# Performance work log

Hardware: AMD Instinct MI355X
Metric: run time of the kernel (lower is better)

Reference implementation:

```python
import jax, jax.numpy as jnp
import numpy as np
import math

B, L, D = 8, 2048, 256


def setup_inputs() -> dict:
    key = jax.random.key(0)
    ks = jax.random.split(key, 8)
    return {
        "query": jax.random.normal(ks[0], (B, L, D), dtype=jnp.float32),
        "key": jax.random.normal(ks[1], (B, L, D), dtype=jnp.float32),
        "value": jax.random.normal(ks[2], (B, L, D), dtype=jnp.float32),
        "mask": jax.random.randint(ks[3], (B, L), 0, 2, dtype=jnp.int32),
        "Wq_w": jax.random.normal(ks[4], (D, D), dtype=jnp.float32) * 0.05,
        "Wq_b": jax.random.normal(ks[5], (D,), dtype=jnp.float32) * 0.05,
        "Wk_w": jax.random.normal(ks[6], (D, D), dtype=jnp.float32) * 0.05,
        "Wk_b": jax.random.normal(ks[7], (D,), dtype=jnp.float32) * 0.05,
    }


def reference(query, key, value, mask, Wq_w, Wq_b, Wk_w, Wk_b):
    d = query.shape[-1]
    q = query @ Wq_w.T + Wq_b            # [B, Lq, D]
    k = key @ Wk_w.T + Wk_b              # [B, Lk, D]
    scores = jnp.einsum("bqd,bkd->bqk", q, k) / math.sqrt(d)  # [B, Lq, Lk]
    m = mask.astype(scores.dtype)[:, None, :]                  # [B, 1, Lk]
    # multiplicative then additive masking, as in original
    scores = jnp.where(m == 0, jnp.asarray(-1e9, scores.dtype), scores * m)
    attn = jax.nn.softmax(scores, axis=-1)
    return jnp.einsum("bqk,bkd->bqd", attn, value)
```

## Files before the change

kernel.cpp:

```cpp
#include <hip/hip_runtime.h>
#include <stdint.h>
#include <stddef.h>

#define B_ 8
#define L_ 2048
#define D_ 256
#define KSPLIT 4
#define KRANGE 512
#define KTILE 32
#define NITER 16

typedef __bf16 bf16x8 __attribute__((ext_vector_type(8)));
typedef float floatx4 __attribute__((ext_vector_type(4)));
typedef float floatx16 __attribute__((ext_vector_type(16)));
typedef _Float16 half4_t __attribute__((ext_vector_type(4)));

__device__ __forceinline__ short f2bf(float f) {
    union { float f; uint32_t u; } v; v.f = f;
    return (short)((v.u + 0x8000u) >> 16);
}

__device__ __forceinline__ uint32_t pack2bf(float a, float b) {
    union { float f; uint32_t u; } x, y; x.f = a; y.f = b;
    return ((x.u + 0x8000u) >> 16) | ((y.u + 0x8000u) & 0xFFFF0000u);
}

__device__ __forceinline__ uint32_t cvtpk_bf16(float lo, float hi2) {
    uint32_t w;
    asm("v_cvt_pk_bf16_f32 %0, %1, %2" : "=v"(w) : "v"(lo), "v"(hi2));
    return w;
}

__device__ __forceinline__ void pl32swap(uint32_t &a, uint32_t &b) {
    asm("v_permlane32_swap_b32 %0, %1" : "+v"(a), "+v"(b));
}

__device__ __forceinline__ void async16(const void* g, void* l) {
    __builtin_amdgcn_global_load_lds(
        (__attribute__((address_space(1))) void*)g,
        (__attribute__((address_space(3))) void*)l,
        16, 0, 0);
}

__global__ __launch_bounds__(256, 3) void prep_kernel(
    const float* __restrict__ Xq, const float* __restrict__ Xk,
    const float* __restrict__ Wq, const float* __restrict__ Wk,
    const float* __restrict__ bq, const float* __restrict__ bk,
    const float* __restrict__ V,
    short* __restrict__ Oq, short* __restrict__ Ok, short* __restrict__ Vt)
{
    __shared__ uint32_t shm[2 * 64 * 20 + 2 * 256 * 20];
    const int bid = blockIdx.x;
    const int tid = threadIdx.x;

    if (bid & 1) {
        uint32_t* T = shm;
        const int vb = bid >> 1;
        const int b  = vb >> 6;
        const int l0 = (vb & 63) * 32;
        const int r2 = tid >> 4;
        const int dg = tid & 15;
        const int lp = r2 ^ ((dg & 3) << 2);
#pragma unroll
        for (int p = 0; p < 4; p++) {
            int d0 = (dg + p * 16) * 4;
            const float* src = V + ((size_t)b * L_ + l0 + r2 * 2) * D_ + d0;
            float4 e0 = *(const float4*)src;
            float4 e1 = *(const float4*)(src + D_);
            T[(d0 + 0) * 20 + lp] = pack2bf(e0.x, e1.x);
            T[(d0 + 1) * 20 + lp] = pack2bf(e0.y, e1.y);
            T[(d0 + 2) * 20 + lp] = pack2bf(e0.z, e1.z);
            T[(d0 + 3) * 20 + lp] = pack2bf(e0.w, e1.w);
        }
        __syncthreads();
#pragma unroll
        for (int p = 0; p < 4; p++) {
            int d = (tid >> 2) + p * 64;
            int c = tid & 3;
            int cp = c ^ ((d >> 2) & 3);
            uint4 u = *(const uint4*)&T[d * 20 + cp * 4];
            *(uint4*)(Vt + ((size_t)b * D_ + d) * L_ + l0 + c * 8) = u;
        }
        return;
    }

    const int pb = bid >> 1;
    const int py = pb >> 8;
    const int px = pb & 255;

    const float* X    = py ? Xk : Xq;
    const float* W    = py ? Wk : Wq;
    const float* bias = py ? bk : bq;
    short* Out        = py ? Ok : Oq;

    uint32_t* As = shm;
    uint32_t* Ws = shm + 2 * 64 * 20;

    const int wid  = tid >> 6;
    const int lane = tid & 63;
    const int m16  = lane & 15;
    const int quad = lane >> 4;
    const int row0 = px * 64;
    const int ar = tid >> 2, cg = tid & 3;

    floatx4 acc[16];
    const floatx4 z4 = {0.f, 0.f, 0.f, 0.f};
#pragma unroll
    for (int i = 0; i < 16; i++) acc[i] = z4;

    {
        const float* srcA = X + (size_t)(row0 + ar) * D_ + cg * 8;
        float4 a = *(const float4*)srcA, b2 = *(const float4*)(srcA + 4);
        uint4 u; u.x = pack2bf(a.x, a.y); u.y = pack2bf(a.z, a.w);
        u.z = pack2bf(b2.x, b2.y); u.w = pack2bf(b2.z, b2.w);
        *(uint4*)&As[ar * 20 + cg * 4] = u;
#pragma unroll
        for (int p = 0; p < 4; p++) {
            const float* srcW = W + (size_t)(p * 64 + ar) * D_ + cg * 8;
            float4 wa = *(const float4*)srcW, wb = *(const float4*)(srcW + 4);
            uint4 w; w.x = pack2bf(wa.x, wa.y); w.y = pack2bf(wa.z, wa.w);
            w.z = pack2bf(wb.x, wb.y); w.w = pack2bf(wb.z, wb.w);
            *(uint4*)&Ws[(p * 64 + ar) * 20 + cg * 4] = w;
        }
    }
    __syncthreads();

    for (int kc = 0; kc < 8; kc++) {
        const int buf = kc & 1;
        float4 na, nb, nwa[4], nwb[4];
        if (kc < 7) {
            const int k1 = (kc + 1) * 32;
            const float* srcA = X + (size_t)(row0 + ar) * D_ + k1 + cg * 8;
            na = *(const float4*)srcA; nb = *(const float4*)(srcA + 4);
#pragma unroll
            for (int p = 0; p < 4; p++) {
                const float* srcW = W + (size_t)(p * 64 + ar) * D_ + k1 + cg * 8;
                nwa[p] = *(const float4*)srcW; nwb[p] = *(const float4*)(srcW + 4);
            }
        }
        bf16x8 af = *(const bf16x8*)&As[buf * 1280 + (wid * 16 + m16) * 20 + quad * 4];
#pragma unroll
        for (int n = 0; n < 16; n++) {
            bf16x8 bfr = *(const bf16x8*)&Ws[buf * 5120 + (n * 16 + m16) * 20 + quad * 4];
            acc[n] = __builtin_amdgcn_mfma_f32_16x16x32_bf16(af, bfr, acc[n], 0, 0, 0);
        }
        if (kc < 7) {
            uint4 u; u.x = pack2bf(na.x, na.y); u.y = pack2bf(na.z, na.w);
            u.z = pack2bf(nb.x, nb.y); u.w = pack2bf(nb.z, nb.w);
            *(uint4*)&As[(buf ^ 1) * 1280 + ar * 20 + cg * 4] = u;
#pragma unroll
            for (int p = 0; p < 4; p++) {
                uint4 w; w.x = pack2bf(nwa[p].x, nwa[p].y); w.y = pack2bf(nwa[p].z, nwa[p].w);
                w.z = pack2bf(nwb[p].x, nwb[p].y); w.w = pack2bf(nwb[p].z, nwb[p].w);
                *(uint4*)&Ws[(buf ^ 1) * 5120 + (p * 64 + ar) * 20 + cg * 4] = w;
            }
        }
        __syncthreads();
    }
#pragma unroll
    for (int n = 0; n < 16; n++) {
        const int col = n * 16 + m16;
        const float bv = bias[col];
#pragma unroll
        for (int r = 0; r < 4; r++) {
            const int row = row0 + wid * 16 + quad * 4 + r;
            Out[(size_t)row * D_ + col] = f2bf(acc[n][r] + bv);
        }
    }
}

__global__ __launch_bounds__(256, 2) void flash_kernel(
    const short* __restrict__ Qb, const short* __restrict__ Kb,
    const short* __restrict__ Vt, const int* __restrict__ mask,
    float* __restrict__ Out, _Float16* __restrict__ Part,
    float* __restrict__ Lpart)
{
    __shared__ short Ks[2][KTILE * 256];
    __shared__ short Vs[2][256 * KTILE];

    const int tid  = threadIdx.x;
    const int wid  = tid >> 6;
    const int lane = tid & 63;
    const int l31  = lane & 31;
    const int hi   = lane >> 5;
    const int b  = blockIdx.x;
    const int q0 = blockIdx.y * 128;
    const int z  = blockIdx.z;

    const char* kgb = (const char*)(Kb + ((size_t)b * L_ + z * KRANGE) * D_);
    const char* vgb = (const char*)(Vt + (size_t)b * D_ * L_ + z * KRANGE);
    const int*  mg  = mask + b * L_ + z * KRANGE;

    bf16x8 qf[16];
    {
        const short* qrow = Qb + ((size_t)b * L_ + q0 + wid * 32 + l31) * D_ + hi * 8;
#pragma unroll
        for (int dt = 0; dt < 16; dt++)
            qf[dt] = *(const bf16x8*)(qrow + dt * 16);
    }

    uint32_t mbits = 0;
#pragma unroll
    for (int t = 0; t < NITER; t++)
        mbits |= (mg[t * KTILE + l31] != 0 ? 1u : 0u) << t;

    floatx16 o[8];
#pragma unroll
    for (int n = 0; n < 8; n++)
#pragma unroll
        for (int r = 0; r < 16; r++) o[n][r] = 0.f;
    float rsum = 0.f;

    const int KBb = l31 * 512 + ((((l31 & 7) ^ ((l31 >> 3) & 3)) ^ hi) << 4);
    const int VBb = l31 * 64 + (((((l31 >> 1) & 3) ^ ((l31 >> 3) & 1)) ^ hi) << 4);

    int koff[4], voff[4];
#pragma unroll
    for (int c = 0; c < 4; c++) {
        int row = wid * 8 + c * 2 + hi;
        int gk = l31 ^ (row & 7) ^ ((row >> 3) & 3);
        koff[c] = row * 512 + gk * 16;
        int d = (wid * 4 + c) * 16 + (lane >> 2);
        int gv = (lane & 3) ^ ((lane >> 3) & 3) ^ ((lane >> 5) & 1);
        voff[c] = d * (L_ * 2) + gv * 16;
    }

#pragma unroll
    for (int c = 0; c < 4; c++)
        async16(kgb + koff[c], &Ks[0][0] + (wid * 4 + c) * 512);
#pragma unroll
    for (int c = 0; c < 4; c++)
        async16(vgb + voff[c], &Vs[1][0] + (wid * 4 + c) * 512);
    __builtin_amdgcn_s_waitcnt(0x0F70);
    __syncthreads();

    const float C2 = 0.09016844f;
    bf16x8 pfA, pfB;
    {
        union { uint32_t u[4]; bf16x8 v; } zz;
        zz.u[0] = 0; zz.u[1] = 0; zz.u[2] = 0; zz.u[3] = 0;
        pfA = zz.v; pfB = zz.v;
    }

    for (int t2 = 0; t2 < NITER; t2 += 2) {
#pragma unroll
        for (int half = 0; half < 2; half++) {
            const int t = t2 + half;
            const int buf = half;

            {
                const char* kp = kgb + (size_t)(t + 1) * (KTILE * D_ * 2);
                const char* vp = vgb + (size_t)t * (KTILE * 2);
#pragma unroll
                for (int c = 0; c < 4; c++)
                    async16(kp + koff[c], &Ks[buf ^ 1][0] + (wid * 4 + c) * 512);
#pragma unroll
                for (int c = 0; c < 4; c++)
                    async16(vp + voff[c], &Vs[buf][0] + (wid * 4 + c) * 512);
            }

            const char* kl = (const char*)&Ks[buf][0];
            floatx16 s0, s1;
#pragma unroll
            for (int r = 0; r < 16; r++) { s0[r] = 0.f; s1[r] = 0.f; }
            __builtin_amdgcn_s_setprio(1);
#pragma unroll
            for (int dt = 0; dt < 16; dt += 2) {
                bf16x8 kf0 = *(const bf16x8*)(kl + (KBb ^ (dt << 5)));
                bf16x8 kf1 = *(const bf16x8*)(kl + (KBb ^ ((dt + 1) << 5)));
                s0 = __builtin_amdgcn_mfma_f32_32x32x16_bf16(kf0, qf[dt], s0, 0, 0, 0);
                s1 = __builtin_amdgcn_mfma_f32_32x32x16_bf16(kf1, qf[dt + 1], s1, 0, 0, 0);
            }

            const char* vl = (const char*)&Vs[buf ^ 1][0];
#pragma unroll
            for (int n = 0; n < 8; n++) {
                bf16x8 vf0 = *(const bf16x8*)(vl + (VBb ^ (n << 11)));
                bf16x8 vf1 = *(const bf16x8*)(vl + (VBb ^ ((n << 11) | 32)));
                o[n] = __builtin_amdgcn_mfma_f32_32x32x16_bf16(pfA, vf0, o[n], 0, 0, 0);
                o[n] = __builtin_amdgcn_mfma_f32_32x32x16_bf16(pfB, vf1, o[n], 0, 0, 0);
            }
            __builtin_amdgcn_s_setprio(0);

            uint32_t mb = (uint32_t)__ballot((mbits >> t) & 1) >> (hi * 4);
            uint32_t w[8];
#pragma unroll
            for (int i = 0; i < 8; i++) {
                const int r0 = 2 * i, r1 = 2 * i + 1;
                const int k0 = (r0 & 3) + 8 * (r0 >> 2);
                float sv0 = s0[r0] + s1[r0];
                float sv1 = s0[r1] + s1[r1];
                float e0 = ((mb >> k0) & 1) ? exp2f(sv0 * C2) : 0.f;
                float e1 = ((mb >> (k0 + 1)) & 1) ? exp2f(sv1 * C2) : 0.f;
                rsum += e0 + e1;
                w[i] = cvtpk_bf16(e0, e1);
            }
            pl32swap(w[0], w[2]); pl32swap(w[1], w[3]);
            pl32swap(w[4], w[6]); pl32swap(w[5], w[7]);
            {
                union { uint32_t u[4]; bf16x8 v; } ua, ub;
                ua.u[0] = w[0]; ua.u[1] = w[1]; ua.u[2] = w[2]; ua.u[3] = w[3];
                ub.u[0] = w[4]; ub.u[1] = w[5]; ub.u[2] = w[6]; ub.u[3] = w[7];
                pfA = ua.v; pfB = ub.v;
            }

            __syncthreads();
        }
    }

    {
        const char* vl = (const char*)&Vs[1][0];
        __builtin_amdgcn_s_setprio(1);
#pragma unroll
        for (int n = 0; n < 8; n++) {
            bf16x8 vf0 = *(const bf16x8*)(vl + (VBb ^ (n << 11)));
            bf16x8 vf1 = *(const bf16x8*)(vl + (VBb ^ ((n << 11) | 32)));
            o[n] = __builtin_amdgcn_mfma_f32_32x32x16_bf16(pfA, vf0, o[n], 0, 0, 0);
            o[n] = __builtin_amdgcn_mfma_f32_32x32x16_bf16(pfB, vf1, o[n], 0, 0, 0);
        }
        __builtin_amdgcn_s_setprio(0);
    }

    rsum += __shfl_xor(rsum, 32);

    const size_t BLD = (size_t)B_ * L_ * D_;
    const size_t rowbase = (size_t)b * L_ + q0 + wid * 32;
    if (z == 0) {
        float* po = Out + rowbase * D_;
#pragma unroll
        for (int n = 0; n < 8; n++)
#pragma unroll
            for (int r = 0; r < 16; r++) {
                int q = (r & 3) + 8 * (r >> 2) + 4 * hi;
                po[(size_t)q * D_ + n * 32 + l31] = o[n][r];
            }
    } else {
        _Float16* pp = Part + (size_t)(z - 1) * BLD + rowbase * D_;
#pragma unroll
        for (int n = 0; n < 8; n++)
#pragma unroll
            for (int r = 0; r < 16; r++) {
                int q = (r & 3) + 8 * (r >> 2) + 4 * hi;
                pp[(size_t)q * D_ + n * 32 + l31] = (_Float16)o[n][r];
            }
    }
    if (lane < 32) {
        Lpart[(size_t)z * (B_ * L_) + rowbase + lane] = rsum;
    }
}

__global__ __launch_bounds__(256) void norm_kernel(
    float* __restrict__ Out, const _Float16* __restrict__ Part,
    const float* __restrict__ Lpart)
{
    const int idx = blockIdx.x * 256 + threadIdx.x;
    const int row = idx >> 6;
    const int c   = (idx & 63) * 4;
    const size_t off = (size_t)row * D_ + c;
    const size_t BLD = (size_t)B_ * L_ * D_;
    float4 acc = *(float4*)(Out + off);
#pragma unroll
    for (int zz = 0; zz < 3; zz++) {
        half4_t h = *(const half4_t*)(Part + zz * BLD + off);
        acc.x += (float)h.x; acc.y += (float)h.y;
        acc.z += (float)h.z; acc.w += (float)h.w;
    }
    const int BL = B_ * L_;
    float l = Lpart[row] + Lpart[BL + row] + Lpart[2 * BL + row] + Lpart[3 * BL + row];
    float inv = 1.0f / l;
    acc.x *= inv; acc.y *= inv; acc.z *= inv; acc.w *= inv;
    *(float4*)(Out + off) = acc;
}

extern "C" void kernel_launch(void* const* d_in, const int* in_sizes, int n_in,
                              void* d_out, int out_size, void* d_ws, size_t ws_size,
                              hipStream_t stream) {
    const float* query = (const float*)d_in[0];
    const float* key   = (const float*)d_in[1];
    const float* value = (const float*)d_in[2];
    const int*   mask  = (const int*)d_in[3];
    const float* Wq_w  = (const float*)d_in[4];
    const float* Wq_b  = (const float*)d_in[5];
    const float* Wk_w  = (const float*)d_in[6];
    const float* Wk_b  = (const float*)d_in[7];
    float* out = (float*)d_out;

    const size_t BLD = (size_t)B_ * L_ * D_;
    short* qb = (short*)d_ws;
    short* kb = qb + BLD;
    short* vt = kb + BLD;
    _Float16* part = (_Float16*)(vt + BLD);
    float* lpart = (float*)(part + 3 * BLD);

    prep_kernel<<<dim3(1024), 256, 0, stream>>>(query, key, Wq_w, Wk_w, Wq_b, Wk_b,
                                                value, qb, kb, vt);
    flash_kernel<<<dim3(8, 16, 4), 256, 0, stream>>>(qb, kb, vt, mask, out, part, lpart);
    norm_kernel<<<dim3((B_ * L_ * D_ / 4) / 256), 256, 0, stream>>>(out, part, lpart);
}
```

Baseline: 199.4 us.

## Use 512-thread flash blocks sharing K/V tiles and split prep into two kernels

```diff
diff --git a/kernel.cpp b/kernel.cpp
--- a/kernel.cpp
+++ b/kernel.cpp
@@ -42,65 +42,26 @@
         16, 0, 0);
 }
 
-__global__ __launch_bounds__(256, 3) void prep_kernel(
+__global__ __launch_bounds__(256, 3) void proj_kernel(
     const float* __restrict__ Xq, const float* __restrict__ Xk,
     const float* __restrict__ Wq, const float* __restrict__ Wk,
     const float* __restrict__ bq, const float* __restrict__ bk,
-    const float* __restrict__ V,
-    short* __restrict__ Oq, short* __restrict__ Ok, short* __restrict__ Vt)
+    short* __restrict__ Oq, short* __restrict__ Ok)
 {
-    __shared__ uint32_t shm[2 * 64 * 20 + 2 * 256 * 20];
-    const int bid = blockIdx.x;
-    const int tid = threadIdx.x;
-
-    if (bid & 1) {
-        uint32_t* T = shm;
-        const int vb = bid >> 1;
-        const int b  = vb >> 6;
-        const int l0 = (vb & 63) * 32;
-        const int r2 = tid >> 4;
-        const int dg = tid & 15;
-        const int lp = r2 ^ ((dg & 3) << 2);
-#pragma unroll
-        for (int p = 0; p < 4; p++) {
-            int d0 = (dg + p * 16) * 4;
-            const float* src = V + ((size_t)b * L_ + l0 + r2 * 2) * D_ + d0;
-            float4 e0 = *(const float4*)src;
-            float4 e1 = *(const float4*)(src + D_);
-            T[(d0 + 0) * 20 + lp] = pack2bf(e0.x, e1.x);
-            T[(d0 + 1) * 20 + lp] = pack2bf(e0.y, e1.y);
-            T[(d0 + 2) * 20 + lp] = pack2bf(e0.z, e1.z);
-            T[(d0 + 3) * 20 + lp] = pack2bf(e0.w, e1.w);
-        }
-        __syncthreads();
-#pragma unroll
-        for (int p = 0; p < 4; p++) {
-            int d = (tid >> 2) + p * 64;
-            int c = tid & 3;
-            int cp = c ^ ((d >> 2) & 3);
-            uint4 u = *(const uint4*)&T[d * 20 + cp * 4];
-            *(uint4*)(Vt + ((size_t)b * D_ + d) * L_ + l0 + c * 8) = u;
-        }
-        return;
-    }
-
-    const int pb = bid >> 1;
-    const int py = pb >> 8;
-    const int px = pb & 255;
-
-    const float* X    = py ? Xk : Xq;
-    const float* W    = py ? Wk : Wq;
-    const float* bias = py ? bk : bq;
-    short* Out        = py ? Ok : Oq;
-
-    uint32_t* As = shm;
-    uint32_t* Ws = shm + 2 * 64 * 20;
-
+    const float* X    = blockIdx.y ? Xk : Xq;
+    const float* W    = blockIdx.y ? Wk : Wq;
+    const float* bias = blockIdx.y ? bk : bq;
+    short* Out        = blockIdx.y ? Ok : Oq;
+
+    __shared__ uint32_t As[2][64 * 20];
+    __shared__ uint32_t Ws[2][256 * 20];
+
+    const int tid  = threadIdx.x;
     const int wid  = tid >> 6;
     const int lane = tid & 63;
     const int m16  = lane & 15;
     const int quad = lane >> 4;
-    const int row0 = px * 64;
+    const int row0 = blockIdx.x * 64;
     const int ar = tid >> 2, cg = tid & 3;
 
     floatx4 acc[16];
@@ -113,14 +74,14 @@
         float4 a = *(const float4*)srcA, b2 = *(const float4*)(srcA + 4);
         uint4 u; u.x = pack2bf(a.x, a.y); u.y = pack2bf(a.z, a.w);
         u.z = pack2bf(b2.x, b2.y); u.w = pack2bf(b2.z, b2.w);
-        *(uint4*)&As[ar * 20 + cg * 4] = u;
+        *(uint4*)&As[0][ar * 20 + cg * 4] = u;
 #pragma unroll
         for (int p = 0; p < 4; p++) {
             const float* srcW = W + (size_t)(p * 64 + ar) * D_ + cg * 8;
             float4 wa = *(const float4*)srcW, wb = *(const float4*)(srcW + 4);
             uint4 w; w.x = pack2bf(wa.x, wa.y); w.y = pack2bf(wa.z, wa.w);
             w.z = pack2bf(wb.x, wb.y); w.w = pack2bf(wb.z, wb.w);
-            *(uint4*)&Ws[(p * 64 + ar) * 20 + cg * 4] = w;
+            *(uint4*)&Ws[0][(p * 64 + ar) * 20 + cg * 4] = w;
         }
     }
     __syncthreads();
@@ -138,21 +99,21 @@
                 nwa[p] = *(const float4*)srcW; nwb[p] = *(const float4*)(srcW + 4);
             }
         }
-        bf16x8 af = *(const bf16x8*)&As[buf * 1280 + (wid * 16 + m16) * 20 + quad * 4];
+        bf16x8 af = *(const bf16x8*)&As[buf][(wid * 16 + m16) * 20 + quad * 4];
 #pragma unroll
         for (int n = 0; n < 16; n++) {
-            bf16x8 bfr = *(const bf16x8*)&Ws[buf * 5120 + (n * 16 + m16) * 20 + quad * 4];
+            bf16x8 bfr = *(const bf16x8*)&Ws[buf][(n * 16 + m16) * 20 + quad * 4];
             acc[n] = __builtin_amdgcn_mfma_f32_16x16x32_bf16(af, bfr, acc[n], 0, 0, 0);
         }
         if (kc < 7) {
             uint4 u; u.x = pack2bf(na.x, na.y); u.y = pack2bf(na.z, na.w);
             u.z = pack2bf(nb.x, nb.y); u.w = pack2bf(nb.z, nb.w);
-            *(uint4*)&As[(buf ^ 1) * 1280 + ar * 20 + cg * 4] = u;
+            *(uint4*)&As[buf ^ 1][ar * 20 + cg * 4] = u;
 #pragma unroll
             for (int p = 0; p < 4; p++) {
                 uint4 w; w.x = pack2bf(nwa[p].x, nwa[p].y); w.y = pack2bf(nwa[p].z, nwa[p].w);
                 w.z = pack2bf(nwb[p].x, nwb[p].y); w.w = pack2bf(nwb[p].z, nwb[p].w);
-                *(uint4*)&Ws[(buf ^ 1) * 5120 + (p * 64 + ar) * 20 + cg * 4] = w;
+                *(uint4*)&Ws[buf ^ 1][(p * 64 + ar) * 20 + cg * 4] = w;
             }
         }
         __syncthreads();
@@ -169,7 +130,39 @@
     }
 }
 
-__global__ __launch_bounds__(256, 2) void flash_kernel(
+__global__ __launch_bounds__(256, 2) void vtrans_kernel(
+    const float* __restrict__ V, short* __restrict__ Vt)
+{
+    __shared__ uint32_t T[256 * 20];
+    const int tid = threadIdx.x;
+    const int b  = blockIdx.y;
+    const int l0 = blockIdx.x * 32;
+    const int r2 = tid >> 4;
+    const int dg = tid & 15;
+    const int lp = r2 ^ ((dg & 3) << 2);
+#pragma unroll
+    for (int p = 0; p < 4; p++) {
+        int d0 = (dg + p * 16) * 4;
+        const float* src = V + ((size_t)b * L_ + l0 + r2 * 2) * D_ + d0;
+        float4 e0 = *(const float4*)src;
+        float4 e1 = *(const float4*)(src + D_);
+        T[(d0 + 0) * 20 + lp] = pack2bf(e0.x, e1.x);
+        T[(d0 + 1) * 20 + lp] = pack2bf(e0.y, e1.y);
+        T[(d0 + 2) * 20 + lp] = pack2bf(e0.z, e1.z);
+        T[(d0 + 3) * 20 + lp] = pack2bf(e0.w, e1.w);
+    }
+    __syncthreads();
+#pragma unroll
+    for (int p = 0; p < 4; p++) {
+        int d = (tid >> 2) + p * 64;
+        int c = tid & 3;
+        int cp = c ^ ((d >> 2) & 3);
+        uint4 u = *(const uint4*)&T[d * 20 + cp * 4];
+        *(uint4*)(Vt + ((size_t)b * D_ + d) * L_ + l0 + c * 8) = u;
+    }
+}
+
+__global__ __launch_bounds__(512, 2) void flash_kernel(
     const short* __restrict__ Qb, const short* __restrict__ Kb,
     const short* __restrict__ Vt, const int* __restrict__ mask,
     float* __restrict__ Out, _Float16* __restrict__ Part,
@@ -184,7 +177,7 @@
     const int l31  = lane & 31;
     const int hi   = lane >> 5;
     const int b  = blockIdx.x;
-    const int q0 = blockIdx.y * 128;
+    const int q0 = blockIdx.y * 256;
     const int z  = blockIdx.z;
 
     const char* kgb = (const char*)(Kb + ((size_t)b * L_ + z * KRANGE) * D_);
@@ -214,23 +207,23 @@
     const int KBb = l31 * 512 + ((((l31 & 7) ^ ((l31 >> 3) & 3)) ^ hi) << 4);
     const int VBb = l31 * 64 + (((((l31 >> 1) & 3) ^ ((l31 >> 3) & 1)) ^ hi) << 4);
 
-    int koff[4], voff[4];
-#pragma unroll
-    for (int c = 0; c < 4; c++) {
-        int row = wid * 8 + c * 2 + hi;
+    int koff[2], voff[2];
+#pragma unroll
+    for (int c = 0; c < 2; c++) {
+        int row = wid * 4 + c * 2 + hi;
         int gk = l31 ^ (row & 7) ^ ((row >> 3) & 3);
         koff[c] = row * 512 + gk * 16;
-        int d = (wid * 4 + c) * 16 + (lane >> 2);
+        int d = (wid * 2 + c) * 16 + (lane >> 2);
         int gv = (lane & 3) ^ ((lane >> 3) & 3) ^ ((lane >> 5) & 1);
         voff[c] = d * (L_ * 2) + gv * 16;
     }
 
 #pragma unroll
-    for (int c = 0; c < 4; c++)
-        async16(kgb + koff[c], &Ks[0][0] + (wid * 4 + c) * 512);
-#pragma unroll
-    for (int c = 0; c < 4; c++)
-        async16(vgb + voff[c], &Vs[1][0] + (wid * 4 + c) * 512);
+    for (int c = 0; c < 2; c++)
+        async16(kgb + koff[c], &Ks[0][0] + (wid * 2 + c) * 512);
+#pragma unroll
+    for (int c = 0; c < 2; c++)
+        async16(vgb + voff[c], &Vs[1][0] + (wid * 2 + c) * 512);
     __builtin_amdgcn_s_waitcnt(0x0F70);
     __syncthreads();
 
@@ -249,14 +242,14 @@
             const int buf = half;
 
             {
-                const char* kp = kgb + (size_t)(t + 1) * (KTILE * D_ * 2);
+                const char* kp = kgb + (size_t)((t + 1) & 15) * (KTILE * D_ * 2);
                 const char* vp = vgb + (size_t)t * (KTILE * 2);
 #pragma unroll
-                for (int c = 0; c < 4; c++)
-                    async16(kp + koff[c], &Ks[buf ^ 1][0] + (wid * 4 + c) * 512);
-#pragma unroll
-                for (int c = 0; c < 4; c++)
-                    async16(vp + voff[c], &Vs[buf][0] + (wid * 4 + c) * 512);
+                for (int c = 0; c < 2; c++)
+                    async16(kp + koff[c], &Ks[buf ^ 1][0] + (wid * 2 + c) * 512);
+#pragma unroll
+                for (int c = 0; c < 2; c++)
+                    async16(vp + voff[c], &Vs[buf][0] + (wid * 2 + c) * 512);
             }
 
             const char* kl = (const char*)&Ks[buf][0];
@@ -392,8 +385,8 @@
     _Float16* part = (_Float16*)(vt + BLD);
     float* lpart = (float*)(part + 3 * BLD);
 
-    prep_kernel<<<dim3(1024), 256, 0, stream>>>(query, key, Wq_w, Wk_w, Wq_b, Wk_b,
-                                                value, qb, kb, vt);
-    flash_kernel<<<dim3(8, 16, 4), 256, 0, stream>>>(qb, kb, vt, mask, out, part, lpart);
+    proj_kernel<<<dim3(256, 2), 256, 0, stream>>>(query, key, Wq_w, Wk_w, Wq_b, Wk_b, qb, kb);
+    vtrans_kernel<<<dim3(64, 8), 256, 0, stream>>>(value, vt);
+    flash_kernel<<<dim3(8, 8, 4), 512, 0, stream>>>(qb, kb, vt, mask, out, part, lpart);
     norm_kernel<<<dim3((B_ * L_ * D_ / 4) / 256), 256, 0, stream>>>(out, part, lpart);
 }
```

Measured after the change: 178.2 us. 10.6% less time.
